# Kernel optimization log

Measured on AMD Instinct MI355X. Metric: run time of the kernel, lower is better.

## Reference

```python
import jax, jax.numpy as jnp
import numpy as np

DIM = 2048
N_HEADS = 16
N_KV = 8
NUM_REP = N_HEADS // N_KV  # 2
HEAD_DIM = DIM // N_HEADS // 2  # 64
EPS = 1e-5
THETA = 10000.0
B, S = 2, 2048


def setup_inputs() -> dict:
    key = jax.random.key(0)
    ks = jax.random.split(key, 12)
    x = jax.random.normal(ks[0], (B, S, DIM), dtype=jnp.float32)
    wq = jax.random.normal(ks[1], (DIM, DIM), dtype=jnp.float32) * 0.02
    wk = jax.random.normal(ks[2], (DIM, DIM // NUM_REP), dtype=jnp.float32) * 0.02
    wv = jax.random.normal(ks[3], (DIM, DIM // NUM_REP), dtype=jnp.float32) * 0.02
    wo = jax.random.normal(ks[4], (DIM, DIM), dtype=jnp.float32) * 0.02
    lambda_q1 = jax.random.normal(ks[5], (HEAD_DIM,), dtype=jnp.float32) * 0.1
    lambda_k1 = jax.random.normal(ks[6], (HEAD_DIM,), dtype=jnp.float32) * 0.1
    lambda_q2 = jax.random.normal(ks[7], (HEAD_DIM,), dtype=jnp.float32) * 0.1
    lambda_k2 = jax.random.normal(ks[8], (HEAD_DIM,), dtype=jnp.float32) * 0.1
    lambda_init = jnp.array([0.8], dtype=jnp.float32)
    subln_w = jnp.ones((2 * HEAD_DIM,), dtype=jnp.float32)
    # rope tables: precompute_freqs_cis(dim=2*HEAD_DIM) then sliced to first HEAD_DIM//2 freqs
    exps = jnp.arange(0, HEAD_DIM, 2, dtype=jnp.float32) / (2.0 * HEAD_DIM)
    freqs = THETA ** (-exps)  # [HEAD_DIM//2]
    ang = jnp.arange(S, dtype=jnp.float32)[:, None] * freqs[None, :]  # [S, HEAD_DIM//2]
    return {
        "x": x, "wq": wq, "wk": wk, "wv": wv, "wo": wo,
        "lambda_q1": lambda_q1, "lambda_k1": lambda_k1,
        "lambda_q2": lambda_q2, "lambda_k2": lambda_k2,
        "lambda_init": lambda_init, "subln_w": subln_w,
        "freqs_cos": jnp.cos(ang), "freqs_sin": jnp.sin(ang),
    }


def _rope(t, cos, sin):
    # t: [B,S,H,hd]; cos/sin: [S, hd//2]; complex-pair rotation on (even, odd)
    e, o = t[..., 0::2], t[..., 1::2]
    c = cos[None, :, None, :]
    s = sin[None, :, None, :]
    return jnp.stack([e * c - o * s, e * s + o * c], axis=-1).reshape(t.shape)


def _repeat_kv_buggy(t, n_rep):
    # faithful to source: t is [B, n_kv, S, hd]; unsqueeze at dim 3 then reshape,
    # which flattens (n_kv, S, rep) -> (n_kv*rep, S)
    b, n_kv, slen, hd = t.shape
    exp = jnp.broadcast_to(t[:, :, :, None, :], (b, n_kv, slen, n_rep, hd))
    return exp.reshape(b, n_kv * n_rep, slen, hd)


def _attn(q, k, v, scale):
    # q,k: [B,H,S,hd]; v: [B,H,S,2hd]
    scores = jnp.einsum('bhqd,bhkd->bhqk', q, k) * scale
    p = jax.nn.softmax(scores, axis=-1)
    return jnp.einsum('bhqk,bhkd->bhqd', p, v)


def reference(x, wq, wk, wv, wo, lambda_q1, lambda_k1, lambda_q2, lambda_k2,
              lambda_init, subln_w, freqs_cos, freqs_sin):
    bsz, seqlen, _ = x.shape
    scale = HEAD_DIM ** -0.5
    q = (x @ wq).reshape(bsz, seqlen, 2 * N_HEADS, HEAD_DIM)
    k = (x @ wk).reshape(bsz, seqlen, 2 * N_KV, HEAD_DIM)
    v = (x @ wv).reshape(bsz, seqlen, N_KV, 2 * HEAD_DIM)
    q = _rope(q, freqs_cos, freqs_sin)
    k = _rope(k, freqs_cos, freqs_sin)
    q = q.reshape(bsz, seqlen, N_HEADS, 2, HEAD_DIM)
    k = k.reshape(bsz, seqlen, N_KV, 2, HEAD_DIM)
    q1 = q[:, :, :, 0].transpose(0, 2, 1, 3)  # [B,H,S,hd]
    q2 = q[:, :, :, 1].transpose(0, 2, 1, 3)
    k1 = _repeat_kv_buggy(k[:, :, :, 0].transpose(0, 2, 1, 3), NUM_REP)
    k2 = _repeat_kv_buggy(k[:, :, :, 1].transpose(0, 2, 1, 3), NUM_REP)
    vr = _repeat_kv_buggy(v.transpose(0, 2, 1, 3), NUM_REP)  # [B,H,S,2hd]
    attn1 = _attn(q1, k1, vr, scale)
    attn2 = _attn(q2, k2, vr, scale)
    lambda_1 = jnp.exp(jnp.sum(lambda_q1 * lambda_k1))
    lambda_2 = jnp.exp(jnp.sum(lambda_q2 * lambda_k2))
    lambda_full = lambda_1 - lambda_2 + lambda_init[0]
    attn = attn1 - lambda_full * attn2  # [B,H,S,2hd]
    # sub-layer RMSNorm over 2*HEAD_DIM
    rms = jax.lax.rsqrt(jnp.mean(attn * attn, axis=-1, keepdims=True) + EPS)
    attn = attn * rms * subln_w
    attn = attn * (1.0 - lambda_init[0])
    attn = attn.transpose(0, 2, 1, 3).reshape(bsz, seqlen, N_HEADS * 2 * HEAD_DIM)
    return attn @ wo
```

## Files before the change

### kernel.cpp

```cpp
#include <hip/hip_runtime.h>
#include <stdint.h>

typedef unsigned short u16;
typedef __attribute__((ext_vector_type(8))) short bf16x8v;
typedef __attribute__((ext_vector_type(4))) float f32x4;

#define DIM   2048
#define NH    16
#define NKV   8
#define HD    64
#define B_    2
#define S_    2048
#define ROWS  (B_*S_)
#define NQKV  4096
#define EPS_   1e-5f
#define SCALE_ 0.125f

__device__ __forceinline__ u16 bfbits(float f) {
  union { float f; unsigned int u; } a; a.f = f;
  unsigned int u = a.u;
  return (u16)((u + 0x7FFFu + ((u >> 16) & 1u)) >> 16);
}

__device__ __forceinline__ f32x4 mfma16(bf16x8v a, bf16x8v b, f32x4 c) {
  return __builtin_amdgcn_mfma_f32_16x16x32_bf16(a, b, c, 0, 0, 0);
}

__device__ __forceinline__ void gload_lds16(const void* g, void* l) {
  __builtin_amdgcn_global_load_lds(
      (const __attribute__((address_space(1))) unsigned int*)g,
      (__attribute__((address_space(3))) unsigned int*)l, 16, 0, 0);
}

__global__ void cast_f32_bf16(const float* __restrict__ src, u16* __restrict__ dst, int n4) {
  int i = blockIdx.x * 256 + threadIdx.x;
  if (i >= n4) return;
  float4 v = ((const float4*)src)[i];
  ushort4 o; o.x = bfbits(v.x); o.y = bfbits(v.y); o.z = bfbits(v.z); o.w = bfbits(v.w);
  ((ushort4*)dst)[i] = o;
}

__global__ void transpose_cast(const float* __restrict__ src, u16* __restrict__ dst, int R, int C) {
  __shared__ float t[32][33];
  int c0 = blockIdx.x * 32, r0 = blockIdx.y * 32;
  int x = threadIdx.x, y = threadIdx.y;
#pragma unroll
  for (int i = 0; i < 4; ++i) t[y + 8*i][x] = src[(size_t)(r0 + y + 8*i) * C + c0 + x];
  __syncthreads();
#pragma unroll
  for (int i = 0; i < 4; ++i) dst[(size_t)(c0 + y + 8*i) * R + r0 + x] = bfbits(t[x][y + 8*i]);
}

__global__ void v_transpose(const float* __restrict__ qkv, u16* __restrict__ Vt) {
  __shared__ float t[32][33];
  int z = blockIdx.z;
  int b = z >> 3, kv = z & 7;
  int s0 = blockIdx.x * 32, d0 = blockIdx.y * 32;
  int x = threadIdx.x, y = threadIdx.y;
  const float* src = qkv + (size_t)b * S_ * NQKV + 3072 + kv * 128;
#pragma unroll
  for (int i = 0; i < 4; ++i) t[y + 8*i][x] = src[(size_t)(s0 + y + 8*i) * NQKV + d0 + x];
  __syncthreads();
  u16* dst = Vt + ((size_t)(b * NKV + kv) * 128) * S_;
#pragma unroll
  for (int i = 0; i < 4; ++i) dst[(size_t)(d0 + y + 8*i) * S_ + s0 + x] = bfbits(t[x][y + 8*i]);
}

__global__ void rope_kernel(const float* __restrict__ qkv, const float* __restrict__ fc,
                            const float* __restrict__ fs, u16* __restrict__ D1, u16* __restrict__ D2,
                            int hshift, int coloff) {
  int p = blockIdx.x * 256 + threadIdx.x;
  int i = p & 31;
  int hh = (p >> 5) & ((1 << hshift) - 1);
  int row = p >> (5 + hshift);
  int s = row & (S_ - 1);
  int b = row >> 11;
  const float* src = qkv + (size_t)row * NQKV + coloff + hh * HD + 2 * i;
  float e = src[0], o = src[1];
  float c = fc[s * 32 + i], sn = fs[s * 32 + i];
  float r0 = e * c - o * sn, r1 = e * sn + o * c;
  u16* dst = (hh & 1) ? D2 : D1;
  int nh = 1 << (hshift - 1);
  size_t offo = (((size_t)b * nh + (hh >> 1)) * S_ + s) * HD + 2 * i;
  unsigned int packed = (unsigned int)bfbits(r0) | ((unsigned int)bfbits(r1) << 16);
  *(unsigned int*)(dst + offo) = packed;
}

__global__ void lambda_kernel(const float* lq1, const float* lk1, const float* lq2,
                              const float* lk2, const float* li, float* scal) {
  int t = threadIdx.x;
  float p1 = lq1[t] * lk1[t];
  float p2 = lq2[t] * lk2[t];
#pragma unroll
  for (int off = 32; off > 0; off >>= 1) { p1 += __shfl_xor(p1, off); p2 += __shfl_xor(p2, off); }
  if (t == 0) {
    scal[0] = __expf(p1) - __expf(p2) + li[0];
    scal[1] = 1.0f - li[0];
  }
}

__global__ __launch_bounds__(256) void gemm_bt(const u16* __restrict__ A, const u16* __restrict__ Bt,
                                               float* __restrict__ C, int M, int N, int K) {
  __shared__ u16 As[128 * 32];
  __shared__ u16 Bs[128 * 32];
  const int tid = threadIdx.x;
  const int wave = tid >> 6, lane = tid & 63;
  const int lr = lane & 15, lk = (lane >> 4) * 8;
  const size_t row0 = (size_t)blockIdx.y * 128, col0 = (size_t)blockIdx.x * 128;
  const int wr = (wave >> 1) * 64, wc = (wave & 1) * 64;
  f32x4 acc[4][4] = {};
  for (int kt = 0; kt < K; kt += 32) {
#pragma unroll
    for (int i = 0; i < 2; ++i) {
      int c = i * 256 + tid;
      int r = c >> 2, c8 = (c & 3) * 8;
      gload_lds16(A  + (row0 + r) * (size_t)K + kt + c8, (char*)As + (i * 256 + wave * 64) * 16);
      gload_lds16(Bt + (col0 + r) * (size_t)K + kt + c8, (char*)Bs + (i * 256 + wave * 64) * 16);
    }
    __syncthreads();
    bf16x8v af[4], bv[4];
#pragma unroll
    for (int m = 0; m < 4; ++m) af[m] = *(const bf16x8v*)(As + (wr + m * 16 + lr) * 32 + lk);
#pragma unroll
    for (int n = 0; n < 4; ++n) bv[n] = *(const bf16x8v*)(Bs + (wc + n * 16 + lr) * 32 + lk);
#pragma unroll
    for (int m = 0; m < 4; ++m)
#pragma unroll
      for (int n = 0; n < 4; ++n) acc[m][n] = mfma16(af[m], bv[n], acc[m][n]);
    __syncthreads();
  }
  const int crow = (lane >> 4) * 4;
#pragma unroll
  for (int m = 0; m < 4; ++m)
#pragma unroll
    for (int n = 0; n < 4; ++n) {
      float* cp = C + (row0 + wr + m * 16 + crow) * (size_t)N + col0 + wc + n * 16 + lr;
#pragma unroll
      for (int j = 0; j < 4; ++j) cp[(size_t)j * N] = acc[m][n][j];
    }
}

__device__ __forceinline__ void attn_step2(const u16* K1, const u16* K2, const u16* Vts,
                                           u16* Pw1, u16* Pw2,
                                           const bf16x8v* q1f, const bf16x8v* q2f,
                                           float* m1, float* l1, f32x4* O1,
                                           float* m2, float* l2, f32x4* O2,
                                           int lane) {
  const int lr = lane & 15, cq = lane >> 4, crow = cq * 4;
  f32x4 s1[4] = {}, s2[4] = {};
  __builtin_amdgcn_s_setprio(1);
#pragma unroll
  for (int kf = 0; kf < 4; ++kf) {
    const int row = kf * 16 + lr, sw = row & 7;
    const bf16x8v ka0 = *(const bf16x8v*)(K1 + row * 64 + ((cq ^ sw) * 8));
    const bf16x8v ka1 = *(const bf16x8v*)(K1 + row * 64 + (((cq + 4) ^ sw) * 8));
    const bf16x8v kb0 = *(const bf16x8v*)(K2 + row * 64 + ((cq ^ sw) * 8));
    const bf16x8v kb1 = *(const bf16x8v*)(K2 + row * 64 + (((cq + 4) ^ sw) * 8));
    s1[kf] = mfma16(q1f[0], ka0, s1[kf]);
    s2[kf] = mfma16(q2f[0], kb0, s2[kf]);
    s1[kf] = mfma16(q1f[1], ka1, s1[kf]);
    s2[kf] = mfma16(q2f[1], kb1, s2[kf]);
  }
  __builtin_amdgcn_s_setprio(0);
  float pm1[4], pm2[4];
#pragma unroll
  for (int j = 0; j < 4; ++j) { pm1[j] = -1e30f; pm2[j] = -1e30f; }
#pragma unroll
  for (int kf = 0; kf < 4; ++kf)
#pragma unroll
    for (int j = 0; j < 4; ++j) {
      float a = s1[kf][j] * SCALE_, b = s2[kf][j] * SCALE_;
      s1[kf][j] = a; s2[kf][j] = b;
      pm1[j] = fmaxf(pm1[j], a); pm2[j] = fmaxf(pm2[j], b);
    }
#pragma unroll
  for (int off = 1; off < 16; off <<= 1)
#pragma unroll
    for (int j = 0; j < 4; ++j) {
      pm1[j] = fmaxf(pm1[j], __shfl_xor(pm1[j], off));
      pm2[j] = fmaxf(pm2[j], __shfl_xor(pm2[j], off));
    }
  float al1[4], al2[4], ps1[4], ps2[4];
#pragma unroll
  for (int j = 0; j < 4; ++j) {
    float mn1 = fmaxf(m1[j], pm1[j]), mn2 = fmaxf(m2[j], pm2[j]);
    al1[j] = __expf(m1[j] - mn1);     al2[j] = __expf(m2[j] - mn2);
    m1[j] = mn1;                      m2[j] = mn2;
    ps1[j] = 0.f;                     ps2[j] = 0.f;
  }
#pragma unroll
  for (int kf = 0; kf < 4; ++kf)
#pragma unroll
    for (int j = 0; j < 4; ++j) {
      float p1 = __expf(s1[kf][j] - m1[j]);
      float p2 = __expf(s2[kf][j] - m2[j]);
      s1[kf][j] = p1; s2[kf][j] = p2;
      ps1[j] += p1;   ps2[j] += p2;
    }
#pragma unroll
  for (int off = 1; off < 16; off <<= 1)
#pragma unroll
    for (int j = 0; j < 4; ++j) {
      ps1[j] += __shfl_xor(ps1[j], off);
      ps2[j] += __shfl_xor(ps2[j], off);
    }
#pragma unroll
  for (int j = 0; j < 4; ++j) {
    l1[j] = l1[j] * al1[j] + ps1[j];
    l2[j] = l2[j] * al2[j] + ps2[j];
  }
#pragma unroll
  for (int f = 0; f < 8; ++f)
#pragma unroll
    for (int j = 0; j < 4; ++j) { O1[f][j] *= al1[j]; O2[f][j] *= al2[j]; }
#pragma unroll
  for (int kf = 0; kf < 4; ++kf) {
    const int ch = kf * 2 + (lr >> 3), cl = lr & 7;
#pragma unroll
    for (int j = 0; j < 4; ++j) {
      const int row = crow + j;
      const int o = row * 64 + ((ch ^ (row & 7)) * 8) + cl;
      Pw1[o] = bfbits(s1[kf][j]);
      Pw2[o] = bfbits(s2[kf][j]);
    }
  }
  __builtin_amdgcn_s_setprio(1);
#pragma unroll
  for (int kst = 0; kst < 2; ++kst) {
    const int po = lr * 64 + (((kst * 4 + cq) ^ (lr & 7)) * 8);
    bf16x8v pf1 = *(const bf16x8v*)(Pw1 + po);
    bf16x8v pf2 = *(const bf16x8v*)(Pw2 + po);
#pragma unroll
    for (int f = 0; f < 8; ++f) {
      const int row = f * 16 + lr;
      bf16x8v vf = *(const bf16x8v*)(Vts + row * 64 + (((kst * 4 + cq) ^ (row & 7)) * 8));
      O1[f] = mfma16(pf1, vf, O1[f]);
      O2[f] = mfma16(pf2, vf, O2[f]);
    }
  }
  __builtin_amdgcn_s_setprio(0);
}

__device__ __forceinline__ void stage_tile(const u16* k1b, const u16* k2b, const u16* vb,
                                           int key0, u16* K1d, u16* K2d, u16* Vd,
                                           int tid, int wave) {
#pragma unroll
  for (int i = 0; i < 2; ++i) {
    int n = i * 256 + tid;
    int r = n >> 3, cl = (n & 7) ^ (r & 7);
    gload_lds16(k1b + (size_t)(key0 + r) * HD + cl * 8, (char*)K1d + (i * 256 + wave * 64) * 16);
    gload_lds16(k2b + (size_t)(key0 + r) * HD + cl * 8, (char*)K2d + (i * 256 + wave * 64) * 16);
  }
#pragma unroll
  for (int i = 0; i < 4; ++i) {
    int n = i * 256 + tid;
    int r = n >> 3, cl = (n & 7) ^ (r & 7);
    gload_lds16(vb + (size_t)r * S_ + key0 + cl * 8, (char*)Vd + (i * 256 + wave * 64) * 16);
  }
}

__global__ __launch_bounds__(256) void attn_kernel(
    const u16* __restrict__ Q1, const u16* __restrict__ Q2,
    const u16* __restrict__ K1g, const u16* __restrict__ K2g,
    const u16* __restrict__ Vt, const float* __restrict__ scal,
    const float* __restrict__ subw, u16* __restrict__ attnb) {
  __shared__ u16 K1s[2][64 * 64];
  __shared__ u16 K2s[2][64 * 64];
  __shared__ u16 Vts[2][128 * 64];
  __shared__ u16 Ps1[4][16 * 64];
  __shared__ u16 Ps2[4][16 * 64];
  const int qb = blockIdx.x, h = blockIdx.y, b = blockIdx.z;
  const int tid = threadIdx.x;
  const int wave = tid >> 6, lane = tid & 63;
  const int lr = lane & 15, lkq = (lane >> 4) * 8;
  const int crow = (lane >> 4) * 4;
  const int kv = h >> 1;
  const int keybase = (h & 1) * 1024;

  const int srow = qb * 64 + wave * 16 + lr;
  const u16* q1p = Q1 + (((size_t)b * NH + h) * S_ + srow) * HD + lkq;
  const u16* q2p = Q2 + (((size_t)b * NH + h) * S_ + srow) * HD + lkq;
  bf16x8v q1f[2], q2f[2];
  q1f[0] = *(const bf16x8v*)(q1p);       q1f[1] = *(const bf16x8v*)(q1p + 32);
  q2f[0] = *(const bf16x8v*)(q2p);       q2f[1] = *(const bf16x8v*)(q2p + 32);

  f32x4 O1[8] = {}, O2[8] = {};
  float m1[4], l1[4], m2[4], l2[4];
#pragma unroll
  for (int j = 0; j < 4; ++j) { m1[j] = -1e30f; l1[j] = 0.f; m2[j] = -1e30f; l2[j] = 0.f; }

  const u16* k1b = K1g + ((size_t)b * NKV + kv) * S_ * HD;
  const u16* k2b = K2g + ((size_t)b * NKV + kv) * S_ * HD;
  const u16* vb  = Vt  + ((size_t)b * NKV + kv) * 128 * S_;

  stage_tile(k1b, k2b, vb, keybase, K1s[0], K2s[0], Vts[0], tid, wave);
  for (int ck = 0; ck < 16; ++ck) {
    const int cur = ck & 1;
    __syncthreads();
    if (ck < 15)
      stage_tile(k1b, k2b, vb, keybase + (ck + 1) * 64,
                 K1s[cur ^ 1], K2s[cur ^ 1], Vts[cur ^ 1], tid, wave);
    attn_step2(K1s[cur], K2s[cur], Vts[cur], Ps1[wave], Ps2[wave],
               q1f, q2f, m1, l1, O1, m2, l2, O2, lane);
  }

  const float lam = scal[0], ofac = scal[1];
  float ssq[4] = {0.f, 0.f, 0.f, 0.f};
#pragma unroll
  for (int f = 0; f < 8; ++f)
#pragma unroll
    for (int j = 0; j < 4; ++j) {
      float cv = O1[f][j] / l1[j] - lam * (O2[f][j] / l2[j]);
      O1[f][j] = cv;
      ssq[j] += cv * cv;
    }
#pragma unroll
  for (int off = 1; off < 16; off <<= 1)
#pragma unroll
    for (int j = 0; j < 4; ++j) ssq[j] += __shfl_xor(ssq[j], off);
  float rs[4];
#pragma unroll
  for (int j = 0; j < 4; ++j) rs[j] = rsqrtf(ssq[j] * (1.f / 128.f) + EPS_) * ofac;
  const size_t rowb = (size_t)b * S_ + qb * 64 + wave * 16 + crow;
#pragma unroll
  for (int f = 0; f < 8; ++f) {
    float sw = subw[f * 16 + lr];
#pragma unroll
    for (int j = 0; j < 4; ++j)
      attnb[(rowb + j) * DIM + h * 128 + f * 16 + lr] = bfbits(O1[f][j] * rs[j] * sw);
  }
}

extern "C" void kernel_launch(void* const* d_in, const int* in_sizes, int n_in,
                              void* d_out, int out_size, void* d_ws, size_t ws_size,
                              hipStream_t stream) {
  const float* x   = (const float*)d_in[0];
  const float* wq  = (const float*)d_in[1];
  const float* wk  = (const float*)d_in[2];
  const float* wv  = (const float*)d_in[3];
  const float* wo  = (const float*)d_in[4];
  const float* lq1 = (const float*)d_in[5];
  const float* lk1 = (const float*)d_in[6];
  const float* lq2 = (const float*)d_in[7];
  const float* lk2 = (const float*)d_in[8];
  const float* li  = (const float*)d_in[9];
  const float* subw= (const float*)d_in[10];
  const float* fc  = (const float*)d_in[11];
  const float* fs  = (const float*)d_in[12];
  float* out = (float*)d_out;

  char* ws = (char*)d_ws;
  size_t off = 0;
  auto alloc = [&](size_t bytes) { char* p = ws + off; off += (bytes + 255) & ~(size_t)255; return p; };
  u16*   xb    = (u16*)alloc((size_t)ROWS * DIM * 2);
  u16*   wqkvT = (u16*)alloc((size_t)NQKV * DIM * 2);
  u16*   woT   = (u16*)alloc((size_t)DIM * DIM * 2);
  float* qkv   = (float*)alloc((size_t)ROWS * NQKV * 4);
  u16*   Q1    = (u16*)alloc((size_t)B_ * NH * S_ * HD * 2);
  u16*   Q2    = (u16*)alloc((size_t)B_ * NH * S_ * HD * 2);
  u16*   K1    = (u16*)alloc((size_t)B_ * NKV * S_ * HD * 2);
  u16*   K2    = (u16*)alloc((size_t)B_ * NKV * S_ * HD * 2);
  u16*   Vt    = (u16*)alloc((size_t)B_ * NKV * 128 * S_ * 2);
  u16*   attnb = (u16*)alloc((size_t)ROWS * DIM * 2);
  float* scal  = (float*)alloc(256);

  cast_f32_bf16<<<ROWS * DIM / 4 / 256, 256, 0, stream>>>(x, xb, ROWS * DIM / 4);
  transpose_cast<<<dim3(64, 64), dim3(32, 8), 0, stream>>>(wq, wqkvT, DIM, DIM);
  transpose_cast<<<dim3(32, 64), dim3(32, 8), 0, stream>>>(wk, wqkvT + (size_t)2048 * DIM, DIM, 1024);
  transpose_cast<<<dim3(32, 64), dim3(32, 8), 0, stream>>>(wv, wqkvT + (size_t)3072 * DIM, DIM, 1024);
  transpose_cast<<<dim3(64, 64), dim3(32, 8), 0, stream>>>(wo, woT, DIM, DIM);

  gemm_bt<<<dim3(NQKV / 128, ROWS / 128), 256, 0, stream>>>(xb, wqkvT, qkv, ROWS, NQKV, DIM);

  rope_kernel<<<ROWS * 32 * 32 / 256, 256, 0, stream>>>(qkv, fc, fs, Q1, Q2, 5, 0);
  rope_kernel<<<ROWS * 16 * 32 / 256, 256, 0, stream>>>(qkv, fc, fs, K1, K2, 4, 2048);
  v_transpose<<<dim3(64, 4, 16), dim3(32, 8), 0, stream>>>(qkv, Vt);
  lambda_kernel<<<1, 64, 0, stream>>>(lq1, lk1, lq2, lk2, li, scal);

  attn_kernel<<<dim3(32, NH, B_), 256, 0, stream>>>(Q1, Q2, K1, K2, Vt, scal, subw, attnb);

  gemm_bt<<<dim3(DIM / 128, ROWS / 128), 256, 0, stream>>>(attnb, woT, out, ROWS, DIM, DIM);
}
```

Before: 537.8 us.

## Replace GEMM with 8-wave double-buffered pipelined kernel using swizzled LDS

Replaces the simple 128x128 single-buffered GEMM with a templated 512-thread kernel using 256xBN tiles, K-step 64, double-buffered LDS and an XOR swizzle to avoid bank conflicts. Global-to-LDS loads for the next stage are interleaved with MFMA quadrants, paced by explicit vmcnt waits and barriers. The QKV projection uses 256x256 tiles and the output projection uses 256x128 tiles. The aim is to hide memory latency and raise data reuse in both projections, at the cost of heavy register use and a fragile hand-written schedule.

```diff
diff --git a/kernel.cpp b/kernel.cpp
--- a/kernel.cpp
+++ b/kernel.cpp
@@ -99,44 +99,127 @@
   }
 }
 
-__global__ __launch_bounds__(256) void gemm_bt(const u16* __restrict__ A, const u16* __restrict__ Bt,
-                                               float* __restrict__ C, int M, int N, int K) {
-  __shared__ u16 As[128 * 32];
-  __shared__ u16 Bs[128 * 32];
+template<int NI>
+__global__ __launch_bounds__(512, 2) void gemm8p(const u16* __restrict__ A, const u16* __restrict__ Bt,
+                                                 float* __restrict__ C, int M, int N, int K) {
+  constexpr int BN = NI * 64;
+  constexpr int BROUNDS = BN / 64;
+  __shared__ u16 Al[2][256 * 64];
+  __shared__ u16 Bl[2][BN * 64];
   const int tid = threadIdx.x;
-  const int wave = tid >> 6, lane = tid & 63;
-  const int lr = lane & 15, lk = (lane >> 4) * 8;
-  const size_t row0 = (size_t)blockIdx.y * 128, col0 = (size_t)blockIdx.x * 128;
-  const int wr = (wave >> 1) * 64, wc = (wave & 1) * 64;
-  f32x4 acc[4][4] = {};
-  for (int kt = 0; kt < K; kt += 32) {
-#pragma unroll
-    for (int i = 0; i < 2; ++i) {
-      int c = i * 256 + tid;
-      int r = c >> 2, c8 = (c & 3) * 8;
-      gload_lds16(A  + (row0 + r) * (size_t)K + kt + c8, (char*)As + (i * 256 + wave * 64) * 16);
-      gload_lds16(Bt + (col0 + r) * (size_t)K + kt + c8, (char*)Bs + (i * 256 + wave * 64) * 16);
-    }
-    __syncthreads();
-    bf16x8v af[4], bv[4];
-#pragma unroll
-    for (int m = 0; m < 4; ++m) af[m] = *(const bf16x8v*)(As + (wr + m * 16 + lr) * 32 + lk);
-#pragma unroll
-    for (int n = 0; n < 4; ++n) bv[n] = *(const bf16x8v*)(Bs + (wc + n * 16 + lr) * 32 + lk);
-#pragma unroll
-    for (int m = 0; m < 4; ++m)
-#pragma unroll
-      for (int n = 0; n < 4; ++n) acc[m][n] = mfma16(af[m], bv[n], acc[m][n]);
-    __syncthreads();
-  }
-  const int crow = (lane >> 4) * 4;
-#pragma unroll
-  for (int m = 0; m < 4; ++m)
-#pragma unroll
-    for (int n = 0; n < 4; ++n) {
-      float* cp = C + (row0 + wr + m * 16 + crow) * (size_t)N + col0 + wc + n * 16 + lr;
-#pragma unroll
-      for (int j = 0; j < 4; ++j) cp[(size_t)j * N] = acc[m][n][j];
+  const int wid = tid >> 6, lane = tid & 63;
+  const int wm = wid >> 2, wn = wid & 3;
+  const int lr = lane & 15, cq = lane >> 4;
+  const size_t row0 = (size_t)blockIdx.y * 256, col0 = (size_t)blockIdx.x * BN;
+
+  f32x4 acc[8][NI];
+#pragma unroll
+  for (int i = 0; i < 8; ++i)
+#pragma unroll
+    for (int j = 0; j < NI; ++j) acc[i][j] = f32x4{0.f, 0.f, 0.f, 0.f};
+
+  bf16x8v a[4][2], b0[NI / 2][2], b1[NI / 2][2];
+
+  auto stageA = [&](int buf, int kt) {
+#pragma unroll
+    for (int rd = 0; rd < 4; ++rd) {
+      int n = rd * 512 + tid;
+      int r = n >> 3, c = (n & 7) ^ (r & 7);
+      gload_lds16(A + (row0 + r) * (size_t)K + kt + c * 8,
+                  (char*)&Al[buf][0] + (rd * 512 + wid * 64) * 16);
+    }
+  };
+  auto stageB = [&](int buf, int kt) {
+#pragma unroll
+    for (int rd = 0; rd < BROUNDS; ++rd) {
+      int n = rd * 512 + tid;
+      int r = n >> 3, c = (n & 7) ^ (r & 7);
+      gload_lds16(Bt + (col0 + r) * (size_t)K + kt + c * 8,
+                  (char*)&Bl[buf][0] + (rd * 512 + wid * 64) * 16);
+    }
+  };
+  auto readA = [&](int buf, int mh) {
+#pragma unroll
+    for (int m2 = 0; m2 < 4; ++m2)
+#pragma unroll
+      for (int ks = 0; ks < 2; ++ks) {
+        int rt = wm * 128 + (mh * 4 + m2) * 16 + lr;
+        a[m2][ks] = *(const bf16x8v*)&Al[buf][rt * 64 + (((ks * 4 + cq) ^ (rt & 7)) * 8)];
+      }
+  };
+  auto readB = [&](int buf, int nh, bf16x8v (&bb)[NI / 2][2]) {
+#pragma unroll
+    for (int n2 = 0; n2 < NI / 2; ++n2)
+#pragma unroll
+      for (int ks = 0; ks < 2; ++ks) {
+        int rt = wn * (NI * 16) + (nh * (NI / 2) + n2) * 16 + lr;
+        bb[n2][ks] = *(const bf16x8v*)&Bl[buf][rt * 64 + (((ks * 4 + cq) ^ (rt & 7)) * 8)];
+      }
+  };
+  auto mfmaq = [&](int mh, int nh, bf16x8v (&bb)[NI / 2][2]) {
+    __builtin_amdgcn_s_barrier();
+    asm volatile("s_waitcnt lgkmcnt(0)" ::: "memory");
+    __builtin_amdgcn_sched_barrier(0);
+    __builtin_amdgcn_s_setprio(1);
+#pragma unroll
+    for (int m2 = 0; m2 < 4; ++m2)
+#pragma unroll
+      for (int n2 = 0; n2 < NI / 2; ++n2)
+#pragma unroll
+        for (int ks = 0; ks < 2; ++ks)
+          acc[mh * 4 + m2][nh * (NI / 2) + n2] =
+              mfma16(a[m2][ks], bb[n2][ks], acc[mh * 4 + m2][nh * (NI / 2) + n2]);
+    __builtin_amdgcn_s_setprio(0);
+    __builtin_amdgcn_s_barrier();
+  };
+  auto vmwait = [&](bool last) {
+    if (last) { asm volatile("s_waitcnt vmcnt(0)" ::: "memory"); }
+    else {
+      if constexpr (NI == 4) { asm volatile("s_waitcnt vmcnt(4)" ::: "memory"); }
+      else                   { asm volatile("s_waitcnt vmcnt(2)" ::: "memory"); }
+    }
+  };
+
+  stageA(0, 0);
+  stageB(0, 0);
+  stageB(1, 64);
+  vmwait(false);
+  __builtin_amdgcn_s_barrier();
+
+  const int NITER = K >> 7;
+  for (int it = 0; it < NITER; ++it) {
+    const int kt = it << 7;
+    const bool nl = (it < NITER - 1);
+    readA(0, 0); readB(0, 0, b0);
+    mfmaq(0, 0, b0);
+    readB(0, 1, b1);
+    stageA(1, kt + 64);
+    mfmaq(0, 1, b1);
+    readA(0, 1);
+    if (nl) stageB(0, kt + 128);
+    mfmaq(1, 1, b1);
+    vmwait(!nl);
+    mfmaq(1, 0, b0);
+    readA(1, 0); readB(1, 0, b0);
+    mfmaq(0, 0, b0);
+    readB(1, 1, b1);
+    if (nl) stageA(0, kt + 128);
+    mfmaq(0, 1, b1);
+    readA(1, 1);
+    if (nl) stageB(1, kt + 192);
+    mfmaq(1, 1, b1);
+    vmwait(!nl);
+    mfmaq(1, 0, b0);
+  }
+
+  const int crow = cq * 4;
+#pragma unroll
+  for (int mi = 0; mi < 8; ++mi)
+#pragma unroll
+    for (int ni = 0; ni < NI; ++ni) {
+      float* cp = C + (row0 + wm * 128 + mi * 16 + crow) * (size_t)N + col0 + wn * (NI * 16) + ni * 16 + lr;
+#pragma unroll
+      for (int j = 0; j < 4; ++j) cp[(size_t)j * N] = acc[mi][ni][j];
     }
 }
 
@@ -370,7 +453,7 @@
   transpose_cast<<<dim3(32, 64), dim3(32, 8), 0, stream>>>(wv, wqkvT + (size_t)3072 * DIM, DIM, 1024);
   transpose_cast<<<dim3(64, 64), dim3(32, 8), 0, stream>>>(wo, woT, DIM, DIM);
 
-  gemm_bt<<<dim3(NQKV / 128, ROWS / 128), 256, 0, stream>>>(xb, wqkvT, qkv, ROWS, NQKV, DIM);
+  gemm8p<4><<<dim3(NQKV / 256, ROWS / 256), 512, 0, stream>>>(xb, wqkvT, qkv, ROWS, NQKV, DIM);
 
   rope_kernel<<<ROWS * 32 * 32 / 256, 256, 0, stream>>>(qkv, fc, fs, Q1, Q2, 5, 0);
   rope_kernel<<<ROWS * 16 * 32 / 256, 256, 0, stream>>>(qkv, fc, fs, K1, K2, 4, 2048);
@@ -379,5 +462,5 @@
 
   attn_kernel<<<dim3(32, NH, B_), 256, 0, stream>>>(Q1, Q2, K1, K2, Vt, scal, subw, attnb);
 
-  gemm_bt<<<dim3(DIM / 128, ROWS / 128), 256, 0, stream>>>(attnb, woT, out, ROWS, DIM, DIM);
-}
+  gemm8p<2><<<dim3(DIM / 128, ROWS / 256), 512, 0, stream>>>(attnb, woT, out, ROWS, DIM, DIM);
+}
```

New measurement: 495.1 us. 1.09x faster.
